# Optimization experiments

Hardware: AMD Instinct MI355X
Metric: run time of the kernel (lower is better)

## Reference

```python
import jax, jax.numpy as jnp
import numpy as np


def setup_inputs() -> dict:
    key = jax.random.key(0)
    k1, k2, k3 = jax.random.split(key, 3)
    B, C2, H, W = 8, 128, 28, 28   # resnet18 layer2 output for 224x224 input
    C3, H3, W3 = 256, 14, 14       # resnet18 layer3 output
    M = 30000                      # memory bank patches (post-coreset)
    f2 = jax.random.normal(k1, (B, C2, H, W), dtype=jnp.float32)
    f3 = jax.random.normal(k2, (B, C3, H3, W3), dtype=jnp.float32)
    memory_bank = jax.random.normal(k3, (M, C2 + C3), dtype=jnp.float32)
    return {"f2": f2, "f3": f3, "memory_bank": memory_bank}


def reference(f2, f3, memory_bank):
    """PatchCore predict: multi-layer embed + brute-force 1-NN euclidean distance.

    f2: [B,C2,H,W] (layer2 feats), f3: [B,C3,H3,W3] (layer3 feats),
    memory_bank: [M, C2+C3]. Returns (patch_scores [B,H,W], img_scores [B]).
    """
    B, C2, H, W = f2.shape
    C3 = f3.shape[1]
    # F.interpolate(..., mode='bilinear', align_corners=False) == jax.image.resize bilinear
    f3_up = jax.image.resize(f3, (B, C3, H, W), method="bilinear")
    emb = jnp.concatenate([f2, f3_up], axis=1)            # [B,C,H,W], C=C2+C3
    C = C2 + C3
    patches = emb.transpose(0, 2, 3, 1).reshape(-1, C)    # [N,C], N=B*H*W
    x_sq = jnp.sum(patches * patches, axis=-1, keepdims=True)      # [N,1]
    m_sq = jnp.sum(memory_bank * memory_bank, axis=-1)[None, :]    # [1,M]
    d2 = x_sq + m_sq - 2.0 * (patches @ memory_bank.T)             # [N,M]
    dists = jnp.sqrt(jnp.maximum(d2, 1e-12))
    nn_dist = jnp.min(dists, axis=1)                               # 1-NN (n_neighbors=1)
    patch_scores = nn_dist.reshape(B, H, W)
    img_scores = jnp.max(patch_scores.reshape(B, -1), axis=1)
    return patch_scores, img_scores
```

## Files before the change

### kernel.cpp

```cpp
#include <hip/hip_runtime.h>
#include <hip/hip_bf16.h>
#include <stdint.h>

typedef float f32x4 __attribute__((ext_vector_type(4)));
typedef short bf16x8 __attribute__((ext_vector_type(8)));

#define NPATCH 6272
#define CTOT   384
#define MBANK  30000
#define MPAD   30080

__global__ __launch_bounds__(256) void prep_patches_kernel(
    const float* __restrict__ f2, const float* __restrict__ f3,
    __hip_bfloat16* __restrict__ A, float* __restrict__ x_sq,
    float* __restrict__ nn_d2)
{
  const int lane = threadIdx.x & 63;
  const int n = blockIdx.x * 4 + (threadIdx.x >> 6);
  if (n >= NPATCH) return;
  const int b = n / 784;
  const int hw = n - b * 784;
  const int h = hw / 28;
  const int w = hw - h * 28;

  int h0, h1, w0i, w1i; float wh0, wh1, ww0, ww1;
  if (h & 1) { int k = h >> 1; h0 = k; h1 = (k + 1 < 14) ? k + 1 : 13; wh0 = 0.75f; wh1 = 0.25f; }
  else       { int k = h >> 1; h0 = (k > 0) ? k - 1 : 0; h1 = k;       wh0 = 0.25f; wh1 = 0.75f; }
  if (w & 1) { int k = w >> 1; w0i = k; w1i = (k + 1 < 14) ? k + 1 : 13; ww0 = 0.75f; ww1 = 0.25f; }
  else       { int k = w >> 1; w0i = (k > 0) ? k - 1 : 0; w1i = k;       ww0 = 0.25f; ww1 = 0.75f; }

  float ssum = 0.f;
  #pragma unroll
  for (int j = 0; j < 6; ++j) {
    const int c = j * 64 + lane;
    float v;
    if (j < 2) {
      v = f2[(((size_t)b * 128 + c) * 28 + h) * 28 + w];
    } else {
      const int c3 = c - 128;
      const float* p = f3 + ((size_t)b * 256 + c3) * 196;
      v = wh0 * (ww0 * p[h0 * 14 + w0i] + ww1 * p[h0 * 14 + w1i]) +
          wh1 * (ww0 * p[h1 * 14 + w0i] + ww1 * p[h1 * 14 + w1i]);
    }
    A[(size_t)n * CTOT + c] = __float2bfloat16(v);
    ssum += v * v;
  }
  #pragma unroll
  for (int off = 32; off; off >>= 1) ssum += __shfl_xor(ssum, off);
  if (lane == 0) { x_sq[n] = ssum; nn_d2[n] = __uint_as_float(0x7f800000u); }
}

__global__ __launch_bounds__(256) void prep_bank_kernel(
    const float* __restrict__ mb, __hip_bfloat16* __restrict__ Bb,
    float* __restrict__ m_sq)
{
  const int lane = threadIdx.x & 63;
  const int m = blockIdx.x * 4 + (threadIdx.x >> 6);
  if (m >= MPAD) return;
  if (m < MBANK) {
    float ssum = 0.f;
    #pragma unroll
    for (int j = 0; j < 6; ++j) {
      const int c = j * 64 + lane;
      const float v = mb[(size_t)m * CTOT + c];
      Bb[(size_t)m * CTOT + c] = __float2bfloat16(v);
      ssum += v * v;
    }
    #pragma unroll
    for (int off = 32; off; off >>= 1) ssum += __shfl_xor(ssum, off);
    if (lane == 0) m_sq[m] = ssum;
  } else {
    #pragma unroll
    for (int j = 0; j < 6; ++j) Bb[(size_t)m * CTOT + j * 64 + lane] = __float2bfloat16(0.f);
    if (lane == 0) m_sq[m] = __uint_as_float(0x7f800000u);
  }
}

__device__ __forceinline__ void gl_lds16(const void* g, void* l) {
  __builtin_amdgcn_global_load_lds(
      (const __attribute__((address_space(1))) uint32_t*)g,
      (__attribute__((address_space(3))) uint32_t*)l, 16, 0, 0);
}

__global__ __launch_bounds__(256) void gemm_min_kernel(
    const __hip_bfloat16* __restrict__ A, const __hip_bfloat16* __restrict__ B,
    const float* __restrict__ x_sq, const float* __restrict__ m_sq,
    float* __restrict__ nn_d2)
{
  __shared__ __align__(16) short As[128 * 64];
  __shared__ __align__(16) short Bs[128 * 64];
  const int tid  = threadIdx.x;
  const int lane = tid & 63;
  const int wid  = tid >> 6;
  const int wr = wid >> 1, wc = wid & 1;
  const int row0 = blockIdx.y * 128;
  const int col0 = blockIdx.x * 128;

  f32x4 acc[4][4];
  #pragma unroll
  for (int i = 0; i < 4; ++i)
    #pragma unroll
    for (int j = 0; j < 4; ++j) acc[i][j] = (f32x4){0.f, 0.f, 0.f, 0.f};

  for (int kt = 0; kt < 6; ++kt) {
    const int k0 = kt * 64;
    #pragma unroll
    for (int j = 0; j < 4; ++j) {
      const int cbase = wid * 256 + j * 64;
      const int chunk = cbase + lane;
      const int r  = chunk >> 3;
      const int kc = (chunk & 7) << 3;
      gl_lds16(A + (size_t)(row0 + r) * CTOT + (k0 + kc), &As[cbase * 8]);
      gl_lds16(B + (size_t)(col0 + r) * CTOT + (k0 + kc), &Bs[cbase * 8]);
    }
    __syncthreads();
    #pragma unroll
    for (int kk = 0; kk < 2; ++kk) {
      const int kl = kk * 32 + (lane >> 4) * 8;
      bf16x8 af[4], bfv[4];
      #pragma unroll
      for (int mi = 0; mi < 4; ++mi)
        af[mi] = *(const bf16x8*)&As[(wr * 64 + mi * 16 + (lane & 15)) * 64 + kl];
      #pragma unroll
      for (int ni = 0; ni < 4; ++ni)
        bfv[ni] = *(const bf16x8*)&Bs[(wc * 64 + ni * 16 + (lane & 15)) * 64 + kl];
      #pragma unroll
      for (int mi = 0; mi < 4; ++mi)
        #pragma unroll
        for (int ni = 0; ni < 4; ++ni)
          acc[mi][ni] = __builtin_amdgcn_mfma_f32_16x16x32_bf16(af[mi], bfv[ni], acc[mi][ni], 0, 0, 0);
    }
    __syncthreads();
  }

  float msq[4];
  #pragma unroll
  for (int ni = 0; ni < 4; ++ni) msq[ni] = m_sq[col0 + wc * 64 + ni * 16 + (lane & 15)];

  #pragma unroll
  for (int mi = 0; mi < 4; ++mi) {
    #pragma unroll
    for (int r = 0; r < 4; ++r) {
      float t = msq[0] - 2.f * acc[mi][0][r];
      #pragma unroll
      for (int ni = 1; ni < 4; ++ni) t = fminf(t, msq[ni] - 2.f * acc[mi][ni][r]);
      t = fminf(t, __shfl_xor(t, 1));
      t = fminf(t, __shfl_xor(t, 2));
      t = fminf(t, __shfl_xor(t, 4));
      t = fminf(t, __shfl_xor(t, 8));
      if ((lane & 15) == 0) {
        const int rg = row0 + wr * 64 + mi * 16 + ((lane >> 4) << 2) + r;
        const float v = fmaxf(t + x_sq[rg], 0.f);
        atomicMin((unsigned int*)&nn_d2[rg], __float_as_uint(v));
      }
    }
  }
}

__global__ __launch_bounds__(256) void finalize_kernel(
    const float* __restrict__ nn_d2, float* __restrict__ out)
{
  const int b = blockIdx.x;
  const int tid = threadIdx.x;
  __shared__ float red[4];
  float lmax = 0.f;
  for (int i = tid; i < 784; i += 256) {
    const float d2 = nn_d2[b * 784 + i];
    const float s = sqrtf(fmaxf(d2, 1e-12f));
    out[b * 784 + i] = s;
    lmax = fmaxf(lmax, s);
  }
  #pragma unroll
  for (int off = 32; off; off >>= 1) lmax = fmaxf(lmax, __shfl_xor(lmax, off));
  if ((tid & 63) == 0) red[tid >> 6] = lmax;
  __syncthreads();
  if (tid == 0)
    out[6272 + b] = fmaxf(fmaxf(red[0], red[1]), fmaxf(red[2], red[3]));
}

extern "C" void kernel_launch(void* const* d_in, const int* in_sizes, int n_in,
                              void* d_out, int out_size, void* d_ws, size_t ws_size,
                              hipStream_t stream)
{
  const float* f2 = (const float*)d_in[0];
  const float* f3 = (const float*)d_in[1];
  const float* mb = (const float*)d_in[2];
  float* out = (float*)d_out;

  uint8_t* ws = (uint8_t*)d_ws;
  __hip_bfloat16* A  = (__hip_bfloat16*)(ws);
  __hip_bfloat16* Bb = (__hip_bfloat16*)(ws + 4816896);
  float* x_sq  = (float*)(ws + 27918336);
  float* m_sq  = (float*)(ws + 27943424);
  float* nn_d2 = (float*)(ws + 28063744);

  hipLaunchKernelGGL(prep_patches_kernel, dim3(NPATCH / 4), dim3(256), 0, stream,
                     f2, f3, A, x_sq, nn_d2);
  hipLaunchKernelGGL(prep_bank_kernel, dim3(MPAD / 4), dim3(256), 0, stream,
                     mb, Bb, m_sq);
  hipLaunchKernelGGL(gemm_min_kernel, dim3(MPAD / 128, NPATCH / 128), dim3(256), 0, stream,
                     A, Bb, x_sq, m_sq, nn_d2);
  hipLaunchKernelGGL(finalize_kernel, dim3(8), dim3(256), 0, stream, nn_d2, out);
}
```

Before: 544.8 us.

## Double-buffer GEMM with 256x256 tiles, swizzled LDS and 512-thread blocks

Reworks the distance GEMM to use 256x256 output tiles with 8 waves, double-buffered LDS staging via global_load_lds, an XOR swizzle to avoid bank conflicts, and split-K phases with setprio around the MFMA bursts. Padding is extended on both the patch and bank dimensions so the tiles divide evenly, with the padded rows masked before the atomic min. The bank prep also moves to float2 loads. This is meant to hide global load latency behind MFMA work and raise reuse per loaded tile. In exchange it uses more LDS and registers per block, does more padded work, and the grid becomes coarse (118x25 blocks), which may hurt occupancy.

```diff
diff --git a/kernel.cpp b/kernel.cpp
--- a/kernel.cpp
+++ b/kernel.cpp
@@ -8,7 +8,9 @@
 #define NPATCH 6272
 #define CTOT   384
 #define MBANK  30000
-#define MPAD   30080
+#define MROWS  6400
+#define NCOLS  30208
+#define NKT    6
 
 __global__ __launch_bounds__(256) void prep_patches_kernel(
     const float* __restrict__ f2, const float* __restrict__ f3,
@@ -17,7 +19,12 @@
 {
   const int lane = threadIdx.x & 63;
   const int n = blockIdx.x * 4 + (threadIdx.x >> 6);
-  if (n >= NPATCH) return;
+  if (n >= MROWS) return;
+  if (n >= NPATCH) {
+    #pragma unroll
+    for (int j = 0; j < 6; ++j) A[(size_t)n * CTOT + j * 64 + lane] = __float2bfloat16(0.f);
+    return;
+  }
   const int b = n / 784;
   const int hw = n - b * 784;
   const int h = hw / 28;
@@ -56,15 +63,18 @@
 {
   const int lane = threadIdx.x & 63;
   const int m = blockIdx.x * 4 + (threadIdx.x >> 6);
-  if (m >= MPAD) return;
+  if (m >= NCOLS) return;
   if (m < MBANK) {
     float ssum = 0.f;
     #pragma unroll
-    for (int j = 0; j < 6; ++j) {
-      const int c = j * 64 + lane;
-      const float v = mb[(size_t)m * CTOT + c];
-      Bb[(size_t)m * CTOT + c] = __float2bfloat16(v);
-      ssum += v * v;
+    for (int j = 0; j < 3; ++j) {
+      const int c = j * 128 + lane * 2;
+      const float2 v = *(const float2*)&mb[(size_t)m * CTOT + c];
+      short2 o;
+      o.x = (short)__bfloat16_as_ushort(__float2bfloat16(v.x));
+      o.y = (short)__bfloat16_as_ushort(__float2bfloat16(v.y));
+      *(short2*)&Bb[(size_t)m * CTOT + c] = o;
+      ssum += v.x * v.x + v.y * v.y;
     }
     #pragma unroll
     for (int off = 32; off; off >>= 1) ssum += __shfl_xor(ssum, off);
@@ -82,55 +92,96 @@
       (__attribute__((address_space(3))) uint32_t*)l, 16, 0, 0);
 }
 
-__global__ __launch_bounds__(256) void gemm_min_kernel(
+__global__ __launch_bounds__(512, 2) void gemm_min_kernel(
     const __hip_bfloat16* __restrict__ A, const __hip_bfloat16* __restrict__ B,
     const float* __restrict__ x_sq, const float* __restrict__ m_sq,
     float* __restrict__ nn_d2)
 {
-  __shared__ __align__(16) short As[128 * 64];
-  __shared__ __align__(16) short Bs[128 * 64];
+  __shared__ __align__(16) short As[2][256 * 64];
+  __shared__ __align__(16) short Bs[2][256 * 64];
   const int tid  = threadIdx.x;
   const int lane = tid & 63;
   const int wid  = tid >> 6;
-  const int wr = wid >> 1, wc = wid & 1;
-  const int row0 = blockIdx.y * 128;
-  const int col0 = blockIdx.x * 128;
-
-  f32x4 acc[4][4];
-  #pragma unroll
-  for (int i = 0; i < 4; ++i)
+  const int wr = wid >> 2;
+  const int wc = wid & 3;
+  const int row0 = blockIdx.y * 256;
+  const int col0 = blockIdx.x * 256;
+
+  f32x4 acc[8][4];
+  #pragma unroll
+  for (int i = 0; i < 8; ++i)
     #pragma unroll
     for (int j = 0; j < 4; ++j) acc[i][j] = (f32x4){0.f, 0.f, 0.f, 0.f};
 
-  for (int kt = 0; kt < 6; ++kt) {
+  auto stage = [&](int kt, int buf) {
     const int k0 = kt * 64;
     #pragma unroll
     for (int j = 0; j < 4; ++j) {
-      const int cbase = wid * 256 + j * 64;
-      const int chunk = cbase + lane;
-      const int r  = chunk >> 3;
-      const int kc = (chunk & 7) << 3;
-      gl_lds16(A + (size_t)(row0 + r) * CTOT + (k0 + kc), &As[cbase * 8]);
-      gl_lds16(B + (size_t)(col0 + r) * CTOT + (k0 + kc), &Bs[cbase * 8]);
-    }
-    __syncthreads();
-    #pragma unroll
-    for (int kk = 0; kk < 2; ++kk) {
-      const int kl = kk * 32 + (lane >> 4) * 8;
-      bf16x8 af[4], bfv[4];
-      #pragma unroll
-      for (int mi = 0; mi < 4; ++mi)
-        af[mi] = *(const bf16x8*)&As[(wr * 64 + mi * 16 + (lane & 15)) * 64 + kl];
+      const int cb = j * 512 + wid * 64;
+      const int c  = cb + lane;
+      const int r  = c >> 3;
+      const int ch = (c & 7) ^ (r & 7);
+      gl_lds16(A + (size_t)(row0 + r) * CTOT + k0 + ch * 8, &As[buf][cb * 8]);
+      gl_lds16(B + (size_t)(col0 + r) * CTOT + k0 + ch * 8, &Bs[buf][cb * 8]);
+    }
+  };
+
+  stage(0, 0);
+  stage(1, 1);
+  asm volatile("s_waitcnt vmcnt(8)" ::: "memory");
+  __builtin_amdgcn_s_barrier();
+
+  const int sw = lane & 7;
+  const int rA = wr * 128 + (lane & 15);
+  const int rB = wc * 64 + (lane & 15);
+  const int kq = lane >> 4;
+
+  #pragma unroll
+  for (int t = 0; t < NKT; ++t) {
+    const int cur = t & 1;
+    const short* lA = As[cur];
+    const short* lB = Bs[cur];
+    const int ch0 = (kq ^ sw) << 4;
+    const int ch1 = ((4 + kq) ^ sw) << 4;
+
+    bf16x8 a0[8], b0[4], a1[8], b1[4];
+    #pragma unroll
+    for (int mi = 0; mi < 8; ++mi)
+      a0[mi] = *(const bf16x8*)((const char*)lA + (rA + mi * 16) * 128 + ch0);
+    #pragma unroll
+    for (int ni = 0; ni < 4; ++ni)
+      b0[ni] = *(const bf16x8*)((const char*)lB + (rB + ni * 16) * 128 + ch0);
+    #pragma unroll
+    for (int mi = 0; mi < 8; ++mi)
+      a1[mi] = *(const bf16x8*)((const char*)lA + (rA + mi * 16) * 128 + ch1);
+    #pragma unroll
+    for (int ni = 0; ni < 4; ++ni)
+      b1[ni] = *(const bf16x8*)((const char*)lB + (rB + ni * 16) * 128 + ch1);
+
+    #pragma unroll
+    for (int mi = 0; mi < 8; ++mi)
       #pragma unroll
       for (int ni = 0; ni < 4; ++ni)
-        bfv[ni] = *(const bf16x8*)&Bs[(wc * 64 + ni * 16 + (lane & 15)) * 64 + kl];
+        acc[mi][ni] = __builtin_amdgcn_mfma_f32_16x16x32_bf16(a0[mi], b0[ni], acc[mi][ni], 0, 0, 0);
+
+    asm volatile("s_waitcnt lgkmcnt(0)" ::: "memory");
+    __builtin_amdgcn_s_barrier();
+    if (t + 2 < NKT) stage(t + 2, cur);
+
+    __builtin_amdgcn_s_setprio(1);
+    #pragma unroll
+    for (int mi = 0; mi < 8; ++mi)
       #pragma unroll
-      for (int mi = 0; mi < 4; ++mi)
-        #pragma unroll
-        for (int ni = 0; ni < 4; ++ni)
-          acc[mi][ni] = __builtin_amdgcn_mfma_f32_16x16x32_bf16(af[mi], bfv[ni], acc[mi][ni], 0, 0, 0);
-    }
-    __syncthreads();
+      for (int ni = 0; ni < 4; ++ni)
+        acc[mi][ni] = __builtin_amdgcn_mfma_f32_16x16x32_bf16(a1[mi], b1[ni], acc[mi][ni], 0, 0, 0);
+    __builtin_amdgcn_s_setprio(0);
+
+    if (t + 2 < NKT) {
+      asm volatile("s_waitcnt vmcnt(8)" ::: "memory");
+    } else {
+      asm volatile("s_waitcnt vmcnt(0)" ::: "memory");
+    }
+    __builtin_amdgcn_s_barrier();
   }
 
   float msq[4];
@@ -138,7 +189,7 @@
   for (int ni = 0; ni < 4; ++ni) msq[ni] = m_sq[col0 + wc * 64 + ni * 16 + (lane & 15)];
 
   #pragma unroll
-  for (int mi = 0; mi < 4; ++mi) {
+  for (int mi = 0; mi < 8; ++mi) {
     #pragma unroll
     for (int r = 0; r < 4; ++r) {
       float t = msq[0] - 2.f * acc[mi][0][r];
@@ -149,9 +200,11 @@
       t = fminf(t, __shfl_xor(t, 4));
       t = fminf(t, __shfl_xor(t, 8));
       if ((lane & 15) == 0) {
-        const int rg = row0 + wr * 64 + mi * 16 + ((lane >> 4) << 2) + r;
-        const float v = fmaxf(t + x_sq[rg], 0.f);
-        atomicMin((unsigned int*)&nn_d2[rg], __float_as_uint(v));
+        const int rg = row0 + wr * 128 + mi * 16 + ((lane >> 4) << 2) + r;
+        if (rg < NPATCH) {
+          const float v = fmaxf(t + x_sq[rg], 0.f);
+          atomicMin((unsigned int*)&nn_d2[rg], __float_as_uint(v));
+        }
       }
     }
   }
@@ -189,16 +242,16 @@
 
   uint8_t* ws = (uint8_t*)d_ws;
   __hip_bfloat16* A  = (__hip_bfloat16*)(ws);
-  __hip_bfloat16* Bb = (__hip_bfloat16*)(ws + 4816896);
-  float* x_sq  = (float*)(ws + 27918336);
-  float* m_sq  = (float*)(ws + 27943424);
-  float* nn_d2 = (float*)(ws + 28063744);
-
-  hipLaunchKernelGGL(prep_patches_kernel, dim3(NPATCH / 4), dim3(256), 0, stream,
+  __hip_bfloat16* Bb = (__hip_bfloat16*)(ws + 4915200);
+  float* x_sq  = (float*)(ws + 28114944);
+  float* m_sq  = (float*)(ws + 28140544);
+  float* nn_d2 = (float*)(ws + 28261376);
+
+  hipLaunchKernelGGL(prep_patches_kernel, dim3(MROWS / 4), dim3(256), 0, stream,
                      f2, f3, A, x_sq, nn_d2);
-  hipLaunchKernelGGL(prep_bank_kernel, dim3(MPAD / 4), dim3(256), 0, stream,
+  hipLaunchKernelGGL(prep_bank_kernel, dim3(NCOLS / 4), dim3(256), 0, stream,
                      mb, Bb, m_sq);
-  hipLaunchKernelGGL(gemm_min_kernel, dim3(MPAD / 128, NPATCH / 128), dim3(256), 0, stream,
+  hipLaunchKernelGGL(gemm_min_kernel, dim3(NCOLS / 256, MROWS / 256), dim3(512), 0, stream,
                      A, Bb, x_sq, m_sq, nn_d2);
   hipLaunchKernelGGL(finalize_kernel, dim3(8), dim3(256), 0, stream, nn_d2, out);
 }
```

Result: faster. 452.5 us (-17.0%).
